# Performance work log

Hardware: AMD Instinct MI355X
Metric: run time of the kernel (lower is better)

## Reference

```python
import jax, jax.numpy as jnp
import numpy as np

EMBED = 64
OUT = 64
KERW = 64
DIM = 3

def setup_inputs() -> dict:
    key = jax.random.key(0)
    ks = jax.random.split(key, 6)
    x = jax.random.normal(ks[0], (8, 4096, EMBED), dtype=jnp.float32)
    grid = jax.random.uniform(ks[1], (8, 4096, DIM), dtype=jnp.float32)
    # DenseNet([dim, ker_width_l, output_size*embed_size], GELU): two Linear layers,
    # GELU between, no activation after the last layer.
    W1 = jax.random.normal(ks[2], (DIM, KERW), dtype=jnp.float32) / np.sqrt(DIM)
    b1 = jnp.zeros((KERW,), dtype=jnp.float32)
    W2 = jax.random.normal(ks[3], (KERW, OUT * EMBED), dtype=jnp.float32) / np.sqrt(KERW)
    b2 = jnp.zeros((OUT * EMBED,), dtype=jnp.float32)
    return {"x": x, "grid": grid, "W1": W1, "b1": b1, "W2": W2, "b2": b2}

def reference(x, grid, W1, b1, W2, b2):
    shape = x.shape
    # generator MLP: grid [.., dim] -> per-point weight [.., embed*out]
    h = jax.nn.gelu(grid @ W1 + b1, approximate=False)
    weight = h @ W2 + b2                              # [B, P, embed*out]
    weight = weight.reshape(-1, EMBED, OUT)           # [N, embed, out]
    xf = x.reshape(-1, shape[-1])                     # [N, embed]
    out = jnp.einsum('bi,bio->bo', xf, weight)        # [N, out]
    return out.reshape(*shape[:-1], OUT)
```

## Files before the change

kernel.cpp:

```cpp
#include <hip/hip_runtime.h>
#include <hip/hip_bf16.h>
#include <hip/hip_fp16.h>

typedef _Float16 f16x8 __attribute__((ext_vector_type(8)));
typedef float f32x4 __attribute__((ext_vector_type(4)));

#define N_PTS 32768
#define NCHUNK 65
#define ROWS 64
#define H_STRIDE 66
#define P_STRIDE 68
#define P_WAVE (ROWS * P_STRIDE)

__global__ void prep_kernel(const float* __restrict__ W2,
                            const float* __restrict__ b2,
                            _Float16* __restrict__ wsB) {
    int t = blockIdx.x * blockDim.x + threadIdx.x;
    if (t >= NCHUNK * 4096) return;
    int j    = t & 7;
    int lane = (t >> 3) & 63;
    int nt   = (t >> 9) & 3;
    int s    = (t >> 11) & 1;
    int c    = t >> 12;
    int kl = s * 32 + ((lane >> 4) << 3) + j;
    int o  = nt * 16 + (lane & 15);
    float v;
    if (c < 64) v = W2[(c * 64 + kl) * 64 + o];
    else        v = b2[kl * 64 + o];
    wsB[t] = (_Float16)v;
}

__global__ __launch_bounds__(256, 2) void main_kernel(
    const float* __restrict__ x, const float* __restrict__ gridp,
    const float* __restrict__ W1, const float* __restrict__ b1,
    const _Float16* __restrict__ wsB, float* __restrict__ out) {

  __shared__ _Float16 h_lds[ROWS][H_STRIDE];
  __shared__ float part[4 * P_WAVE];

  const int tid  = threadIdx.x;
  const int lane = tid & 63;
  const int wave = tid >> 6;
  const int rowblk = blockIdx.x * ROWS;

  {
    int row = tid >> 2;
    int kb  = (tid & 3) * 16;
    int r = rowblk + row;
    float g0 = gridp[r * 3 + 0], g1 = gridp[r * 3 + 1], g2 = gridp[r * 3 + 2];
    #pragma unroll 4
    for (int k = kb; k < kb + 16; ++k) {
      float v = g0 * W1[k] + g1 * W1[64 + k] + g2 * W1[128 + k] + b1[k];
      float h = 0.5f * v * (1.0f + erff(v * 0.7071067811865476f));
      h_lds[row][k] = (_Float16)h;
    }
    if ((tid & 3) == 3) h_lds[row][64] = (_Float16)1.0f;
  }
  __syncthreads();

  const int mrow = lane & 15;
  const int kgrp = lane >> 4;

  f16x8 xf[4][2];
  #pragma unroll
  for (int m = 0; m < 4; ++m) {
    #pragma unroll
    for (int s = 0; s < 2; ++s) {
      const float* xp = x + (rowblk + m * 16 + mrow) * 64 + s * 32 + kgrp * 8;
      f16x8 v;
      #pragma unroll
      for (int j = 0; j < 8; ++j) v[j] = (_Float16)xp[j];
      xf[m][s] = v;
    }
  }

  f32x4 acc[4][4];
  #pragma unroll
  for (int m = 0; m < 4; ++m)
    #pragma unroll
    for (int n = 0; n < 4; ++n)
      acc[m][n] = (f32x4){0.f, 0.f, 0.f, 0.f};

  const _Float16* bp = wsB + lane * 8;

  auto LOADB = [&](f16x8* b, int c) {
    #pragma unroll
    for (int q = 0; q < 8; ++q)
      b[q] = *(const f16x8*)(bp + (c * 8 + q) * 512);
  };
  auto COMPUTE = [&](const f16x8* b, int c) {
    #pragma unroll
    for (int m = 0; m < 4; ++m) {
      _Float16 hh = h_lds[m * 16 + mrow][c];
      f16x8 hs = {hh, hh, hh, hh, hh, hh, hh, hh};
      f16x8 a0 = xf[m][0] * hs;
      f16x8 a1 = xf[m][1] * hs;
      #pragma unroll
      for (int n = 0; n < 4; ++n) {
        acc[m][n] = __builtin_amdgcn_mfma_f32_16x16x32_f16(a0, b[n],     acc[m][n], 0, 0, 0);
        acc[m][n] = __builtin_amdgcn_mfma_f32_16x16x32_f16(a1, b[4 + n], acc[m][n], 0, 0, 0);
      }
    }
  };

  const int nch = (wave == 0) ? 17 : 16;
  f16x8 bufA[8], bufB[8];
  LOADB(bufA, wave);
  int i = 1;
  for (; i + 1 < nch; i += 2) {
    LOADB(bufB, wave + 4 * i);
    COMPUTE(bufA, wave + 4 * (i - 1));
    LOADB(bufA, wave + 4 * (i + 1));
    COMPUTE(bufB, wave + 4 * i);
  }
  if (i < nch) {
    LOADB(bufB, wave + 4 * i);
    COMPUTE(bufA, wave + 4 * (i - 1));
    COMPUTE(bufB, wave + 4 * i);
  } else {
    COMPUTE(bufA, wave + 4 * (nch - 1));
  }

  {
    float* pw = part + wave * P_WAVE;
    #pragma unroll
    for (int m = 0; m < 4; ++m)
      #pragma unroll
      for (int n = 0; n < 4; ++n)
        #pragma unroll
        for (int r = 0; r < 4; ++r)
          pw[(m * 16 + kgrp * 4 + r) * P_STRIDE + n * 16 + mrow] = acc[m][n][r];
  }
  __syncthreads();

  {
    int row = tid >> 2;
    int cb  = (tid & 3) * 16;
    const float* p0 = part + row * P_STRIDE + cb;
    float* op = out + (rowblk + row) * 64 + cb;
    #pragma unroll
    for (int j = 0; j < 4; ++j) {
      f32x4 s = *(const f32x4*)(p0 + j * 4);
      #pragma unroll
      for (int w = 1; w < 4; ++w)
        s += *(const f32x4*)(p0 + w * P_WAVE + j * 4);
      *(f32x4*)(op + j * 4) = s;
    }
  }
}

extern "C" void kernel_launch(void* const* d_in, const int* in_sizes, int n_in,
                              void* d_out, int out_size, void* d_ws, size_t ws_size,
                              hipStream_t stream) {
  const float* x    = (const float*)d_in[0];
  const float* grid = (const float*)d_in[1];
  const float* W1   = (const float*)d_in[2];
  const float* b1   = (const float*)d_in[3];
  const float* W2   = (const float*)d_in[4];
  const float* b2   = (const float*)d_in[5];
  float* out = (float*)d_out;
  _Float16* wsB = (_Float16*)d_ws;

  hipLaunchKernelGGL(prep_kernel, dim3((NCHUNK * 4096 + 255) / 256), dim3(256), 0, stream,
                     W2, b2, wsB);
  hipLaunchKernelGGL(main_kernel, dim3(N_PTS / ROWS), dim3(256), 0, stream,
                     x, grid, W1, b1, wsB, out);
}
```

Before: 32.74 us.

## Split chunk loop across 8 waves per block and restructure partial-sum reduction

Doubles the block to 512 threads so each wave handles about half as many K-chunks. Partial sums are now reduced in two LDS phases: waves 0-3 write and waves 4-7 accumulate into 4 buffers. The prep kernel now reads W2 coalesced and scatters into the swizzled layout, and the GELU stage uses vector loads of W1/b1. The aim is more parallel MFMA work per row block and shorter per-wave serial chains, at the cost of extra barriers, a second LDS pass and higher register pressure under launch_bounds(512,4).

```diff
diff --git a/kernel.cpp b/kernel.cpp
--- a/kernel.cpp
+++ b/kernel.cpp
@@ -8,35 +8,30 @@
 #define N_PTS 32768
 #define NCHUNK 65
 #define ROWS 64
-#define H_STRIDE 66
-#define P_STRIDE 68
-#define P_WAVE (ROWS * P_STRIDE)
+#define P_STRIDE 65
+#define P_BUF (ROWS * P_STRIDE)
 
 __global__ void prep_kernel(const float* __restrict__ W2,
                             const float* __restrict__ b2,
                             _Float16* __restrict__ wsB) {
     int t = blockIdx.x * blockDim.x + threadIdx.x;
     if (t >= NCHUNK * 4096) return;
-    int j    = t & 7;
-    int lane = (t >> 3) & 63;
-    int nt   = (t >> 9) & 3;
-    int s    = (t >> 11) & 1;
-    int c    = t >> 12;
-    int kl = s * 32 + ((lane >> 4) << 3) + j;
-    int o  = nt * 16 + (lane & 15);
-    float v;
-    if (c < 64) v = W2[(c * 64 + kl) * 64 + o];
-    else        v = b2[kl * 64 + o];
-    wsB[t] = (_Float16)v;
+    int kk = t >> 6, o = t & 63;
+    float v = (kk < 4096) ? W2[t] : b2[t - 4096 * 64];
+    int c = kk >> 6, kl = kk & 63;
+    int s = kl >> 5, j = kl & 7;
+    int lane = (((kl >> 3) & 3) << 4) | (o & 15);
+    int nt = o >> 4;
+    wsB[(((c * 2 + s) * 4 + nt) * 64 + lane) * 8 + j] = (_Float16)v;
 }
 
-__global__ __launch_bounds__(256, 2) void main_kernel(
+__global__ __launch_bounds__(512, 4) void main_kernel(
     const float* __restrict__ x, const float* __restrict__ gridp,
     const float* __restrict__ W1, const float* __restrict__ b1,
     const _Float16* __restrict__ wsB, float* __restrict__ out) {
 
-  __shared__ _Float16 h_lds[ROWS][H_STRIDE];
-  __shared__ float part[4 * P_WAVE];
+  __shared__ _Float16 h_lds[ROWS][66];
+  __shared__ float part[4][P_BUF];
 
   const int tid  = threadIdx.x;
   const int lane = tid & 63;
@@ -44,17 +39,23 @@
   const int rowblk = blockIdx.x * ROWS;
 
   {
-    int row = tid >> 2;
-    int kb  = (tid & 3) * 16;
+    int row = tid >> 3;
+    int kb  = (tid & 7) * 8;
     int r = rowblk + row;
     float g0 = gridp[r * 3 + 0], g1 = gridp[r * 3 + 1], g2 = gridp[r * 3 + 2];
-    #pragma unroll 4
-    for (int k = kb; k < kb + 16; ++k) {
-      float v = g0 * W1[k] + g1 * W1[64 + k] + g2 * W1[128 + k] + b1[k];
+    f32x4 wa0 = *(const f32x4*)(W1 + kb),       wa1 = *(const f32x4*)(W1 + kb + 4);
+    f32x4 wb0 = *(const f32x4*)(W1 + 64 + kb),  wb1 = *(const f32x4*)(W1 + 64 + kb + 4);
+    f32x4 wc0 = *(const f32x4*)(W1 + 128 + kb), wc1 = *(const f32x4*)(W1 + 128 + kb + 4);
+    f32x4 bb0 = *(const f32x4*)(b1 + kb),       bb1 = *(const f32x4*)(b1 + kb + 4);
+    #pragma unroll
+    for (int q = 0; q < 8; ++q) {
+      float v = (q < 4)
+        ? g0 * wa0[q] + g1 * wb0[q] + g2 * wc0[q] + bb0[q]
+        : g0 * wa1[q - 4] + g1 * wb1[q - 4] + g2 * wc1[q - 4] + bb1[q - 4];
       float h = 0.5f * v * (1.0f + erff(v * 0.7071067811865476f));
-      h_lds[row][k] = (_Float16)h;
+      h_lds[row][kb + q] = (_Float16)h;
     }
-    if ((tid & 3) == 3) h_lds[row][64] = (_Float16)1.0f;
+    if ((tid & 7) == 7) h_lds[row][64] = (_Float16)1.0f;
   }
   __syncthreads();
 
@@ -103,26 +104,28 @@
     }
   };
 
-  const int nch = (wave == 0) ? 17 : 16;
+  const int nch = (wave == 0) ? 9 : 8;
   f16x8 bufA[8], bufB[8];
   LOADB(bufA, wave);
   int i = 1;
   for (; i + 1 < nch; i += 2) {
-    LOADB(bufB, wave + 4 * i);
-    COMPUTE(bufA, wave + 4 * (i - 1));
-    LOADB(bufA, wave + 4 * (i + 1));
-    COMPUTE(bufB, wave + 4 * i);
+    LOADB(bufB, wave + 8 * i);
+    COMPUTE(bufA, wave + 8 * (i - 1));
+    LOADB(bufA, wave + 8 * (i + 1));
+    COMPUTE(bufB, wave + 8 * i);
   }
   if (i < nch) {
-    LOADB(bufB, wave + 4 * i);
-    COMPUTE(bufA, wave + 4 * (i - 1));
-    COMPUTE(bufB, wave + 4 * i);
+    LOADB(bufB, wave + 8 * i);
+    COMPUTE(bufA, wave + 8 * (i - 1));
+    COMPUTE(bufB, wave + 8 * i);
   } else {
-    COMPUTE(bufA, wave + 4 * (nch - 1));
+    COMPUTE(bufA, wave + 8 * (nch - 1));
   }
 
-  {
-    float* pw = part + wave * P_WAVE;
+  __syncthreads();
+
+  if (wave < 4) {
+    float* pw = part[wave];
     #pragma unroll
     for (int m = 0; m < 4; ++m)
       #pragma unroll
@@ -133,19 +136,32 @@
   }
   __syncthreads();
 
+  if (wave >= 4) {
+    float* pw = part[wave - 4];
+    #pragma unroll
+    for (int m = 0; m < 4; ++m)
+      #pragma unroll
+      for (int n = 0; n < 4; ++n)
+        #pragma unroll
+        for (int r = 0; r < 4; ++r)
+          pw[(m * 16 + kgrp * 4 + r) * P_STRIDE + n * 16 + mrow] += acc[m][n][r];
+  }
+  __syncthreads();
+
   {
-    int row = tid >> 2;
-    int cb  = (tid & 3) * 16;
-    const float* p0 = part + row * P_STRIDE + cb;
+    int row = tid >> 3;
+    int cb  = (tid & 7) * 8;
+    const float* p0 = part[0] + row * P_STRIDE + cb;
+    float s[8];
+    #pragma unroll
+    for (int j = 0; j < 8; ++j) s[j] = p0[j];
+    #pragma unroll
+    for (int w = 1; w < 4; ++w)
+      #pragma unroll
+      for (int j = 0; j < 8; ++j) s[j] += p0[w * P_BUF + j];
     float* op = out + (rowblk + row) * 64 + cb;
-    #pragma unroll
-    for (int j = 0; j < 4; ++j) {
-      f32x4 s = *(const f32x4*)(p0 + j * 4);
-      #pragma unroll
-      for (int w = 1; w < 4; ++w)
-        s += *(const f32x4*)(p0 + w * P_WAVE + j * 4);
-      *(f32x4*)(op + j * 4) = s;
-    }
+    *(f32x4*)(op)     = (f32x4){s[0], s[1], s[2], s[3]};
+    *(f32x4*)(op + 4) = (f32x4){s[4], s[5], s[6], s[7]};
   }
 }
 
@@ -163,6 +179,6 @@
 
   hipLaunchKernelGGL(prep_kernel, dim3((NCHUNK * 4096 + 255) / 256), dim3(256), 0, stream,
                      W2, b2, wsB);
-  hipLaunchKernelGGL(main_kernel, dim3(N_PTS / ROWS), dim3(256), 0, stream,
+  hipLaunchKernelGGL(main_kernel, dim3(N_PTS / ROWS), dim3(512), 0, stream,
                      x, grid, W1, b1, wsB, out);
 }
```

After: 112.0 us. 242% more time.

## Coalesce x and W2 loads via LDS staging and vectorize h writes

Applied to the files above, without the earlier changes.

The prep kernel now reads each W2 chunk with coalesced contiguous loads into LDS and writes the MFMA-swizzled fp16 layout out as vector stores. The main kernel loads x with coalesced float4 reads, converts it to fp16 in an LDS region aliased onto the partial-sum buffer, and then reads the MFMA fragments from LDS. It also issues the first B-chunk prefetch earlier, writes the GELU hidden values as 8-wide vector stores, and drops the min-2-blocks launch bound. A barrier is added before the partial-sum writes so the aliased LDS can be reused safely, at the cost of one extra sync per block.

```diff
diff --git a/kernel.cpp b/kernel.cpp
--- a/kernel.cpp
+++ b/kernel.cpp
@@ -8,71 +8,115 @@
 #define N_PTS 32768
 #define NCHUNK 65
 #define ROWS 64
-#define H_STRIDE 66
+#define H_STRIDE 72
+#define X_STRIDE 72
 #define P_STRIDE 68
-#define P_WAVE (ROWS * P_STRIDE)
-
-__global__ void prep_kernel(const float* __restrict__ W2,
-                            const float* __restrict__ b2,
-                            _Float16* __restrict__ wsB) {
-    int t = blockIdx.x * blockDim.x + threadIdx.x;
-    if (t >= NCHUNK * 4096) return;
-    int j    = t & 7;
-    int lane = (t >> 3) & 63;
-    int nt   = (t >> 9) & 3;
-    int s    = (t >> 11) & 1;
-    int c    = t >> 12;
-    int kl = s * 32 + ((lane >> 4) << 3) + j;
-    int o  = nt * 16 + (lane & 15);
-    float v;
-    if (c < 64) v = W2[(c * 64 + kl) * 64 + o];
-    else        v = b2[kl * 64 + o];
-    wsB[t] = (_Float16)v;
+
+__global__ __launch_bounds__(256) void prep_kernel(
+    const float* __restrict__ W2, const float* __restrict__ b2,
+    _Float16* __restrict__ wsB) {
+  __shared__ _Float16 w_lds[64][X_STRIDE];
+  const int c   = blockIdx.x;
+  const int tid = threadIdx.x;
+  {
+    const float* src = (c < 64) ? (W2 + c * 4096 + tid * 16) : (b2 + tid * 16);
+    int kl = tid >> 2, o = (tid & 3) * 16;
+    f16x8 v0, v1;
+    #pragma unroll
+    for (int j = 0; j < 8; ++j) {
+      v0[j] = (_Float16)src[j];
+      v1[j] = (_Float16)src[8 + j];
+    }
+    *(f16x8*)(&w_lds[kl][o])     = v0;
+    *(f16x8*)(&w_lds[kl][o + 8]) = v1;
+  }
+  __syncthreads();
+  #pragma unroll
+  for (int u = 0; u < 2; ++u) {
+    int t = tid + u * 256;
+    int q = t >> 6, lane = t & 63;
+    int klbase = (q >> 2) * 32 + ((lane >> 4) & 3) * 8;
+    int o      = (q & 3) * 16 + (lane & 15);
+    f16x8 v;
+    #pragma unroll
+    for (int j = 0; j < 8; ++j) v[j] = w_lds[klbase + j][o];
+    *(f16x8*)(wsB + c * 4096 + t * 8) = v;
+  }
 }
 
-__global__ __launch_bounds__(256, 2) void main_kernel(
+__global__ __launch_bounds__(256) void main_kernel(
     const float* __restrict__ x, const float* __restrict__ gridp,
     const float* __restrict__ W1, const float* __restrict__ b1,
     const _Float16* __restrict__ wsB, float* __restrict__ out) {
 
   __shared__ _Float16 h_lds[ROWS][H_STRIDE];
-  __shared__ float part[4 * P_WAVE];
+  __shared__ float part[4][ROWS * P_STRIDE];
+  _Float16* x_lds = (_Float16*)&part[0][0];
 
   const int tid  = threadIdx.x;
   const int lane = tid & 63;
   const int wave = tid >> 6;
   const int rowblk = blockIdx.x * ROWS;
 
+  const float* xsrc = x + rowblk * 64 + tid * 16;
+  f32x4 xr0 = *(const f32x4*)(xsrc);
+  f32x4 xr1 = *(const f32x4*)(xsrc + 4);
+  f32x4 xr2 = *(const f32x4*)(xsrc + 8);
+  f32x4 xr3 = *(const f32x4*)(xsrc + 12);
+
   {
     int row = tid >> 2;
     int kb  = (tid & 3) * 16;
     int r = rowblk + row;
     float g0 = gridp[r * 3 + 0], g1 = gridp[r * 3 + 1], g2 = gridp[r * 3 + 2];
-    #pragma unroll 4
-    for (int k = kb; k < kb + 16; ++k) {
+    f16x8 h0, h1;
+    #pragma unroll
+    for (int q = 0; q < 16; ++q) {
+      int k = kb + q;
       float v = g0 * W1[k] + g1 * W1[64 + k] + g2 * W1[128 + k] + b1[k];
       float h = 0.5f * v * (1.0f + erff(v * 0.7071067811865476f));
-      h_lds[row][k] = (_Float16)h;
-    }
+      if (q < 8) h0[q] = (_Float16)h; else h1[q - 8] = (_Float16)h;
+    }
+    *(f16x8*)(&h_lds[row][kb])     = h0;
+    *(f16x8*)(&h_lds[row][kb + 8]) = h1;
     if ((tid & 3) == 3) h_lds[row][64] = (_Float16)1.0f;
+  }
+
+  {
+    int row = tid >> 2, o = (tid & 3) * 16;
+    f16x8 v0, v1;
+    #pragma unroll
+    for (int j = 0; j < 4; ++j) {
+      v0[j]     = (_Float16)xr0[j];
+      v0[4 + j] = (_Float16)xr1[j];
+      v1[j]     = (_Float16)xr2[j];
+      v1[4 + j] = (_Float16)xr3[j];
+    }
+    *(f16x8*)(&x_lds[row * X_STRIDE + o])     = v0;
+    *(f16x8*)(&x_lds[row * X_STRIDE + o + 8]) = v1;
   }
   __syncthreads();
 
   const int mrow = lane & 15;
   const int kgrp = lane >> 4;
 
+  const _Float16* bp = wsB + lane * 8;
+
+  auto LOADB = [&](f16x8* b, int c) {
+    #pragma unroll
+    for (int q = 0; q < 8; ++q)
+      b[q] = *(const f16x8*)(bp + (c * 8 + q) * 512);
+  };
+
+  f16x8 bufA[8], bufB[8];
+  LOADB(bufA, wave);
+
   f16x8 xf[4][2];
   #pragma unroll
-  for (int m = 0; m < 4; ++m) {
-    #pragma unroll
-    for (int s = 0; s < 2; ++s) {
-      const float* xp = x + (rowblk + m * 16 + mrow) * 64 + s * 32 + kgrp * 8;
-      f16x8 v;
-      #pragma unroll
-      for (int j = 0; j < 8; ++j) v[j] = (_Float16)xp[j];
-      xf[m][s] = v;
-    }
-  }
+  for (int m = 0; m < 4; ++m)
+    #pragma unroll
+    for (int s = 0; s < 2; ++s)
+      xf[m][s] = *(const f16x8*)(&x_lds[(m * 16 + mrow) * X_STRIDE + s * 32 + kgrp * 8]);
 
   f32x4 acc[4][4];
   #pragma unroll
@@ -81,13 +125,6 @@
     for (int n = 0; n < 4; ++n)
       acc[m][n] = (f32x4){0.f, 0.f, 0.f, 0.f};
 
-  const _Float16* bp = wsB + lane * 8;
-
-  auto LOADB = [&](f16x8* b, int c) {
-    #pragma unroll
-    for (int q = 0; q < 8; ++q)
-      b[q] = *(const f16x8*)(bp + (c * 8 + q) * 512);
-  };
   auto COMPUTE = [&](const f16x8* b, int c) {
     #pragma unroll
     for (int m = 0; m < 4; ++m) {
@@ -104,8 +141,6 @@
   };
 
   const int nch = (wave == 0) ? 17 : 16;
-  f16x8 bufA[8], bufB[8];
-  LOADB(bufA, wave);
   int i = 1;
   for (; i + 1 < nch; i += 2) {
     LOADB(bufB, wave + 4 * i);
@@ -121,8 +156,10 @@
     COMPUTE(bufA, wave + 4 * (nch - 1));
   }
 
-  {
-    float* pw = part + wave * P_WAVE;
+  __syncthreads();
+
+  {
+    float* pw = part[wave];
     #pragma unroll
     for (int m = 0; m < 4; ++m)
       #pragma unroll
@@ -136,14 +173,14 @@
   {
     int row = tid >> 2;
     int cb  = (tid & 3) * 16;
-    const float* p0 = part + row * P_STRIDE + cb;
+    const float* p0 = part[0] + row * P_STRIDE + cb;
     float* op = out + (rowblk + row) * 64 + cb;
     #pragma unroll
     for (int j = 0; j < 4; ++j) {
       f32x4 s = *(const f32x4*)(p0 + j * 4);
       #pragma unroll
       for (int w = 1; w < 4; ++w)
-        s += *(const f32x4*)(p0 + w * P_WAVE + j * 4);
+        s += *(const f32x4*)(p0 + w * (ROWS * P_STRIDE) + j * 4);
       *(f32x4*)(op + j * 4) = s;
     }
   }
@@ -161,7 +198,7 @@
   float* out = (float*)d_out;
   _Float16* wsB = (_Float16*)d_ws;
 
-  hipLaunchKernelGGL(prep_kernel, dim3((NCHUNK * 4096 + 255) / 256), dim3(256), 0, stream,
+  hipLaunchKernelGGL(prep_kernel, dim3(NCHUNK), dim3(256), 0, stream,
                      W2, b2, wsB);
   hipLaunchKernelGGL(main_kernel, dim3(N_PTS / ROWS), dim3(256), 0, stream,
                      x, grid, W1, b1, wsB, out);
```

After: 33.09 us. Within noise of the previous version (+1.1%).
